# Kernel optimization log

Hardware: AMD Instinct MI355X
Metric: run time of the kernel (lower is better)

## Reference

```python
import jax, jax.numpy as jnp
import numpy as np

DIM = 768
HEADS = 12
HEAD_DIM = DIM // HEADS
SCALE = HEAD_DIM ** -0.5
LN_EPS = 1e-5


def setup_inputs() -> dict:
    key = jax.random.key(0)
    ks = jax.random.split(key, 12)
    B, N, C = 8, 1024, DIM
    g = (6.0 / (C + 3 * C)) ** 0.5  # xavier_uniform bound for qkv
    gp = (6.0 / (C + C)) ** 0.5     # xavier_uniform bound for proj
    return {
        "x": jax.random.normal(ks[0], (B, N, C), jnp.float32),
        "w_qkv_id": jax.random.uniform(ks[1], (3 * C, C), jnp.float32, -g, g),
        "w_qkv_cloth": jax.random.uniform(ks[2], (3 * C, C), jnp.float32, -g, g),
        "w_proj_id": jax.random.uniform(ks[3], (C, C), jnp.float32, -gp, gp),
        "b_proj_id": jnp.zeros((C,), jnp.float32),
        "w_proj_cloth": jax.random.uniform(ks[4], (C, C), jnp.float32, -gp, gp),
        "b_proj_cloth": jnp.zeros((C,), jnp.float32),
        "ln_id_w": jnp.ones((C,), jnp.float32),
        "ln_id_b": jnp.zeros((C,), jnp.float32),
        "ln_cloth_w": jnp.ones((C,), jnp.float32),
        "ln_cloth_b": jnp.zeros((C,), jnp.float32),
        "orth_scale": jnp.asarray(0.1, jnp.float32),
    }


def _layernorm(x, w, b):
    mu = jnp.mean(x, axis=-1, keepdims=True)
    var = jnp.var(x, axis=-1, keepdims=True)
    return (x - mu) * jax.lax.rsqrt(var + LN_EPS) * w + b


def _split_heads(qkv, B, N):
    qkv = qkv.reshape(B, N, 3, HEADS, HEAD_DIM).transpose(2, 0, 3, 1, 4)
    return qkv[0], qkv[1], qkv[2]


def _attn(q, k, v):
    s = jnp.einsum("bhnd,bhmd->bhnm", q, k) * SCALE
    s = jnp.clip(s, -20.0, 20.0)
    a = jax.nn.softmax(s, axis=-1)
    a = jnp.where(jnp.isnan(a), jnp.zeros_like(a), a)  # nan guard (dropout = eval/identity)
    return jnp.einsum("bhnm,bhmd->bhnd", a, v)


def reference(x, w_qkv_id, w_qkv_cloth, w_proj_id, b_proj_id, w_proj_cloth,
              b_proj_cloth, ln_id_w, ln_id_b, ln_cloth_w, ln_cloth_b, orth_scale):
    B, N, C = x.shape
    q_id, k_id, v_id = _split_heads(x @ w_qkv_id.T, B, N)
    q_cl, k_cl, v_cl = _split_heads(x @ w_qkv_cloth.T, B, N)

    # Gram-Schmidt orthogonal projection of q_id against q_cloth
    dot = jnp.sum(q_id * q_cl, axis=-1, keepdims=True)          # [B,H,N,1]
    norm_sq = jnp.sum(q_cl * q_cl, axis=-1, keepdims=True) + 1e-5
    coeff = jnp.clip(dot / norm_sq, -1.0, 1.0)
    scale = jnp.clip(orth_scale, 0.0, 1.0)
    q_id_ortho = q_id - scale * (coeff * q_cl)
    saliency = jnp.clip(jnp.mean(jnp.abs(dot) / jnp.sqrt(norm_sq), axis=1), 0.0, 1.0)  # [B,N,1]

    out_id = _attn(q_id_ortho, k_id, v_id).transpose(0, 2, 1, 3).reshape(B, N, C)
    out_cl = _attn(q_cl, k_cl, v_cl).transpose(0, 2, 1, 3).reshape(B, N, C)

    id_feat = _layernorm(out_id @ w_proj_id.T + b_proj_id, ln_id_w, ln_id_b)
    cl_feat = _layernorm(out_cl @ w_proj_cloth.T + b_proj_cloth, ln_cloth_w, ln_cloth_b)
    return id_feat, cl_feat, saliency
```

## Files before the change

kernel.cpp:

```cpp
#include <hip/hip_runtime.h>

typedef unsigned short u16;
typedef short s16x8 __attribute__((ext_vector_type(8)));
typedef float f32x4 __attribute__((ext_vector_type(4)));

#define DEV __device__ __forceinline__

#if __has_builtin(__builtin_amdgcn_exp2f)
#define EXP2F(x) __builtin_amdgcn_exp2f(x)
#else
#define EXP2F(x) exp2f(x)
#endif

DEV u16 f2bf(float f) {
  unsigned int u = __float_as_uint(f);
  u = (u + 0x7fffu + ((u >> 16) & 1u)) >> 16;
  return (u16)u;
}
DEV float bf2f(u16 h) { return __uint_as_float(((unsigned int)h) << 16); }
DEV unsigned int pk_trunc(float lo, float hi) {
  return __builtin_amdgcn_perm(__float_as_uint(hi), __float_as_uint(lo), 0x07060302u);
}

DEV void g2l16(const void* g, void* l) {
  __builtin_amdgcn_global_load_lds(
      (const __attribute__((address_space(1))) unsigned int*)g,
      (__attribute__((address_space(3))) unsigned int*)l, 16, 0, 0);
}

#define SPLANE 6291456

#define BAR __builtin_amdgcn_s_barrier()
#define WAIT_VM(n) asm volatile("s_waitcnt vmcnt(" #n ")" ::: "memory")
#define WAIT_LGKM0 asm volatile("s_waitcnt lgkmcnt(0)" ::: "memory")
#define PRIO1 __builtin_amdgcn_s_setprio(1)
#define PRIO0 __builtin_amdgcn_s_setprio(0)

__global__ __launch_bounds__(256) void k_cvt(const float* __restrict__ x,
                                             const float* __restrict__ wqi,
                                             const float* __restrict__ wqc,
                                             const float* __restrict__ wpi,
                                             const float* __restrict__ wpc,
                                             u16* __restrict__ xb,
                                             u16* __restrict__ wqkv,
                                             u16* __restrict__ wproj) {
  int i = blockIdx.x * 256 + threadIdx.x;
  const float* src; u16* dst; int off;
  if (i < 1572864)      { src = x;   dst = xb;             off = 0; }
  else if (i < 2015232) { src = wqi; dst = wqkv;           off = 1572864; }
  else if (i < 2457600) { src = wqc; dst = wqkv + 1769472; off = 2015232; }
  else if (i < 2605056) { src = wpi; dst = wproj;          off = 2457600; }
  else                  { src = wpc; dst = wproj + 589824; off = 2605056; }
  int j = i - off;
  float4 v = ((const float4*)src)[j];
  ushort4 o;
  o.x = f2bf(v.x); o.y = f2bf(v.y); o.z = f2bf(v.z); o.w = f2bf(v.w);
  ((ushort4*)dst)[j] = o;
}


DEV void qstg(const u16* pX, const u16* pW, int koff, u16* lA, u16* lB, int wave) {
#pragma unroll
  for (int it = 0; it < 4; ++it) {
    int rb = wave * 32 + it * 8;
    g2l16(pX + koff + it * (8 * 768), &lA[rb * 64]);
    g2l16(pW + koff + it * (8 * 768), &lB[rb * 64]);
  }
}

DEV void qcomp(const u16* lA, const u16* lB, int wr, int wc, int fr, int fq,
               f32x4 (&acc)[4][4]) {
#pragma unroll
  for (int ks = 0; ks < 2; ++ks) {
    s16x8 af[4], bfr[4];
#pragma unroll
    for (int i = 0; i < 4; i++) {
      int row = wc + i * 16 + fr;
      af[i] = *(const s16x8*)&lB[row * 64 + (((ks * 4 + fq) ^ (row & 7)) * 8)];
    }
#pragma unroll
    for (int j = 0; j < 4; j++) {
      int row = wr + j * 16 + fr;
      bfr[j] = *(const s16x8*)&lA[row * 64 + (((ks * 4 + fq) ^ (row & 7)) * 8)];
    }
    PRIO1;
#pragma unroll
    for (int i = 0; i < 4; i++)
#pragma unroll
      for (int j = 0; j < 4; j++)
        acc[i][j] = __builtin_amdgcn_mfma_f32_16x16x32_bf16(af[i], bfr[j], acc[i][j], 0, 0, 0);
    PRIO0;
  }
}

__global__ __launch_bounds__(256, 2) void k_qkv_gemm(const u16* __restrict__ X,
                                                     const u16* __restrict__ Wq,
                                                     u16* __restrict__ QK,
                                                     u16* __restrict__ VT) {
  __shared__ __align__(16) u16 sm[32768];

  const int idx = blockIdx.x;
  const int swz = (idx & 7) * 288 + (idx >> 3);
  const int bx = swz % 18;
  const int rem = swz / 18;
  const int by = rem & 63;
  const int z = rem >> 6;
  const int n0 = bx * 128, m0 = by * 128;

  const int tid = threadIdx.x;
  const int wave = tid >> 6, lane = tid & 63;
  const int wr = (wave >> 1) * 64, wc = (wave & 1) * 64;
  const int fr = lane & 15, fq = lane >> 4;

  const int srow = lane >> 3;
  const int scol = ((lane & 7) ^ srow) * 8;

  const u16* pX = X + (size_t)(m0 + wave * 32 + srow) * 768 + scol;
  const u16* pW = Wq + (size_t)z * (2304 * 768) + (size_t)(n0 + wave * 32 + srow) * 768 + scol;

  u16* const lA0 = sm;
  u16* const lB0 = sm + 8192;
  u16* const lA1 = sm + 16384;
  u16* const lB1 = sm + 24576;

  f32x4 acc[4][4];
#pragma unroll
  for (int i = 0; i < 4; i++)
#pragma unroll
    for (int j = 0; j < 4; j++) acc[i][j] = (f32x4){0.f, 0.f, 0.f, 0.f};

  qstg(pX, pW, 0, lA0, lB0, wave);
  qstg(pX, pW, 64, lA1, lB1, wave);
  WAIT_VM(8);
  BAR;

  const u16* pX2 = pX + 128;
  const u16* pW2 = pW + 128;

#pragma unroll
  for (int ii = 0; ii < 6; ++ii) {
    qcomp(lA0, lB0, wr, wc, fr, fq, acc);
    BAR;
    if (ii < 5) {
      qstg(pX2, pW2, 0, lA0, lB0, wave);
      WAIT_VM(8);
    } else {
      WAIT_VM(0);
    }
    BAR;
    qcomp(lA1, lB1, wr, wc, fr, fq, acc);
    BAR;
    if (ii < 5) {
      qstg(pX2, pW2, 64, lA1, lB1, wave);
      WAIT_VM(8);
      pX2 += 128; pW2 += 128;
    }
    BAR;
  }

  __syncthreads();
  u16* ep = sm + wave * 4608;
#pragma unroll
  for (int i = 0; i < 4; i++)
#pragma unroll
    for (int j = 0; j < 4; j++) {
      unsigned int lo = (unsigned int)f2bf(acc[i][j][0]) | ((unsigned int)f2bf(acc[i][j][1]) << 16);
      unsigned int hi = (unsigned int)f2bf(acc[i][j][2]) | ((unsigned int)f2bf(acc[i][j][3]) << 16);
      uint2 pk; pk.x = lo; pk.y = hi;
      *(uint2*)&ep[(j * 16 + fr) * 72 + i * 16 + fq * 4] = pk;
    }
  __builtin_amdgcn_s_waitcnt(0);

  const int c0 = n0 + wc;
  const int t0 = m0 + wr;
  const int b = t0 >> 10, tt0 = t0 & 1023;
  if (c0 < 1536) {
    const int three = (c0 >= 768) ? 1 : 0;
    const int h = (c0 - three * 768) >> 6;
    u16* dst = QK + ((size_t)z * 2 + three) * SPLANE +
               ((size_t)(b * 12 + h) * 1024 + tt0) * 64;
#pragma unroll
    for (int pass = 0; pass < 8; ++pass) {
      int row = pass * 8 + (lane >> 3);
      int dch = (lane & 7) * 8;
      *(uint4*)&dst[(size_t)row * 64 + dch] = *(const uint4*)&ep[row * 72 + dch];
    }
  } else {
    const int h = (c0 - 1536) >> 6;
    u16* dst = VT + (size_t)z * SPLANE + ((size_t)(b * 12 + h) * 64) * 1024 + tt0;
#pragma unroll
    for (int pass = 0; pass < 8; ++pass) {
      int d = pass * 8 + (lane >> 3);
      int tch = (lane & 7) * 8;
      unsigned int w0[4];
#pragma unroll
      for (int k2 = 0; k2 < 4; k2++) {
        unsigned int lo = ep[(tch + k2 * 2) * 72 + d];
        unsigned int hi = ep[(tch + k2 * 2 + 1) * 72 + d];
        w0[k2] = lo | (hi << 16);
      }
      uint4 val;
      val.x = w0[0]; val.y = w0[1]; val.z = w0[2]; val.w = w0[3];
      *(uint4*)&dst[(size_t)d * 1024 + tch] = val;
    }
  }
}

__global__ __launch_bounds__(256) void k_ortho(u16* __restrict__ QK,
                                               const float* __restrict__ orth_scale,
                                               float* __restrict__ sal) {
  const int wave = threadIdx.x >> 6, lane = threadIdx.x & 63;
  const int row = blockIdx.x * 4 + wave;
  const int b = row >> 10, n = row & 1023;
  const float scale = fminf(fmaxf(orth_scale[0], 0.f), 1.f);
  u16* qid = QK;
  u16* qcl = QK + (size_t)2 * SPLANE;
  float sacc = 0.f;
  for (int h = 0; h < 12; ++h) {
    size_t off = (((size_t)(b * 12 + h)) * 1024 + n) * 64 + lane;
    float qi = bf2f(qid[off]);
    float qc = bf2f(qcl[off]);
    float d = qi * qc, nq = qc * qc;
#pragma unroll
    for (int s = 1; s < 64; s <<= 1) { d += __shfl_xor(d, s); nq += __shfl_xor(nq, s); }
    nq += 1e-5f;
    float coeff = fminf(fmaxf(d / nq, -1.f), 1.f);
    qid[off] = f2bf(qi - scale * coeff * qc);
    sacc += fabsf(d) / sqrtf(nq);
  }
  if (lane == 0) sal[row] = fminf(fmaxf(sacc * (1.f / 12.f), 0.f), 1.f);
}

#define AST 72
#define PST 40
__global__ __launch_bounds__(256, 3) void k_attn(const u16* __restrict__ QK,
                                                 const u16* __restrict__ VT,
                                                 u16* __restrict__ aout) {
  __shared__ __align__(16) u16 sm[19456];
  u16* lK = sm;
  u16* lVT = sm + 4608;
  const int lid = blockIdx.x;
  const int swz = (lid & 7) * 96 + (lid >> 3);
  const int qb = swz & 3;
  const int pr = swz >> 2;
  const int z = pr / 96, bh = pr - (pr / 96) * 96;
  const int q0 = qb * 256;
  const int b = bh / 12, hd = bh - b * 12;
  const size_t plane = (size_t)bh * 65536;
  const u16* Q  = QK + (size_t)z * 2 * SPLANE + plane;
  const u16* K  = QK + ((size_t)z * 2 + 1) * SPLANE + plane;
  const u16* Vt = VT + (size_t)z * SPLANE + plane;

  const int tid = threadIdx.x, wave = tid >> 6, lane = tid & 63;
  const int fr = lane & 15, fq = lane >> 4;
  u16* lP = sm + 9216 + wave * 2560;

  s16x8 qf[4][2];
#pragma unroll
  for (int s = 0; s < 4; s++) {
    const u16* qrow = Q + (size_t)(q0 + wave * 64 + s * 16 + fr) * 64;
    qf[s][0] = *(const s16x8*)&qrow[fq * 8];
    qf[s][1] = *(const s16x8*)&qrow[32 + fq * 8];
  }

  f32x4 oacc[4][4];
  float lsum[4];
#pragma unroll
  for (int s = 0; s < 4; s++) {
    lsum[s] = 0.f;
#pragma unroll
    for (int j = 0; j < 4; j++) oacc[s][j] = (f32x4){0.f, 0.f, 0.f, 0.f};
  }

  const int srow = tid >> 3, sc8 = (tid & 7) * 8;

  uint4 rk0 = *(const uint4*)&K[(size_t)srow * 64 + sc8];
  uint4 rk1 = *(const uint4*)&K[(size_t)(srow + 32) * 64 + sc8];
  uint4 rv0 = *(const uint4*)&Vt[(size_t)srow * 1024 + sc8];
  uint4 rv1 = *(const uint4*)&Vt[(size_t)(srow + 32) * 1024 + sc8];

  for (int kv0 = 0; kv0 < 1024; kv0 += 64) {
    __syncthreads();
    *(uint4*)&lK[srow * AST + sc8]         = rk0;
    *(uint4*)&lK[(srow + 32) * AST + sc8]  = rk1;
    *(uint4*)&lVT[srow * AST + sc8]        = rv0;
    *(uint4*)&lVT[(srow + 32) * AST + sc8] = rv1;
    __syncthreads();

    {
      int nxt = (kv0 + 64) & 1023;
      const u16* kb = K + (size_t)nxt * 64;
      rk0 = *(const uint4*)&kb[(size_t)srow * 64 + sc8];
      rk1 = *(const uint4*)&kb[(size_t)(srow + 32) * 64 + sc8];
      const u16* vb = Vt + nxt;
      rv0 = *(const uint4*)&vb[(size_t)srow * 1024 + sc8];
      rv1 = *(const uint4*)&vb[(size_t)(srow + 32) * 1024 + sc8];
    }

#pragma unroll
    for (int ph = 0; ph < 2; ++ph) {
#pragma unroll
      for (int jh = 0; jh < 2; ++jh) {
        const int jt = ph * 2 + jh;
        s16x8 kf0 = *(const s16x8*)&lK[(jt * 16 + fr) * AST + fq * 8];
        s16x8 kf1 = *(const s16x8*)&lK[(jt * 16 + fr) * AST + 32 + fq * 8];
#pragma unroll
        for (int s = 0; s < 4; s++) {
          f32x4 t = (f32x4){0.f, 0.f, 0.f, 0.f};
          t = __builtin_amdgcn_mfma_f32_16x16x32_bf16(kf0, qf[s][0], t, 0, 0, 0);
          t = __builtin_amdgcn_mfma_f32_16x16x32_bf16(kf1, qf[s][1], t, 0, 0, 0);
          float p0 = EXP2F(fmaf(t[0], 0.18033688f, -28.8539008f));
          float p1 = EXP2F(fmaf(t[1], 0.18033688f, -28.8539008f));
          float p2 = EXP2F(fmaf(t[2], 0.18033688f, -28.8539008f));
          float p3 = EXP2F(fmaf(t[3], 0.18033688f, -28.8539008f));
          lsum[s] += (p0 + p1) + (p2 + p3);
          uint2 pk; pk.x = pk_trunc(p0, p1); pk.y = pk_trunc(p2, p3);
          *(uint2*)&lP[(s * 16 + fr) * PST + jh * 16 + fq * 4] = pk;
        }
      }
      WAIT_LGKM0;
      s16x8 pa[4];
#pragma unroll
      for (int s = 0; s < 4; s++) pa[s] = *(const s16x8*)&lP[(s * 16 + fr) * PST + fq * 8];
#pragma unroll
      for (int jt = 0; jt < 4; jt++) {
        s16x8 vb = *(const s16x8*)&lVT[(jt * 16 + fr) * AST + ph * 32 + fq * 8];
#pragma unroll
        for (int s = 0; s < 4; s++)
          oacc[s][jt] = __builtin_amdgcn_mfma_f32_16x16x32_bf16(pa[s], vb, oacc[s][jt], 0, 0, 0);
      }
    }
  }

#pragma unroll
  for (int s = 0; s < 4; s++) {
    float v = lsum[s];
    v += __shfl_xor(v, 16);
    v += __shfl_xor(v, 32);
    lsum[s] = v;
  }
#pragma unroll
  for (int s = 0; s < 4; s++) {
#pragma unroll
    for (int r = 0; r < 4; r++) {
      float inv = 1.f / __shfl(lsum[s], fq * 4 + r);
      int t = q0 + wave * 64 + s * 16 + fq * 4 + r;
      size_t base = ((size_t)z * 8192 + b * 1024 + t) * 768 + hd * 64 + fr;
#pragma unroll
      for (int jt = 0; jt < 4; jt++)
        aout[base + jt * 16] = f2bf(oacc[s][jt][r] * inv);
    }
  }
}

__global__ __launch_bounds__(256) void k_proj_gemm(const u16* __restrict__ A,
                                                   const u16* __restrict__ Wp,
                                                   const float* __restrict__ bias_id,
                                                   const float* __restrict__ bias_cl,
                                                   u16* __restrict__ out) {
  __shared__ __align__(16) u16 sm[18432];
  u16* lA = sm;
  u16* lB = sm + 8192;
  const int idx = blockIdx.x;
  const int swz = (idx & 7) * 96 + (idx >> 3);
  const int bx = swz % 6;
  const int rem = swz / 6;
  const int by = rem & 63;
  const int z = rem >> 6;
  const int n0 = bx * 128, m0 = by * 128;
  const u16* Az = A + (size_t)z * 8192 * 768;
  const u16* Wz = Wp + (size_t)z * 768 * 768;
  const float* bias = z ? bias_cl : bias_id;
  u16* oz = out + (size_t)z * 8192 * 768;
  const int tid = threadIdx.x;
  const int wave = tid >> 6, lane = tid & 63;
  const int wr = (wave >> 1) * 64, wc = (wave & 1) * 64;
  const int fr = lane & 15, fq = lane >> 4;

  float bv[4][4];
#pragma unroll
  for (int i = 0; i < 4; i++)
#pragma unroll
    for (int r = 0; r < 4; r++) bv[i][r] = bias[n0 + wc + i * 16 + fq * 4 + r];

  f32x4 acc[4][4];
#pragma unroll
  for (int i = 0; i < 4; i++)
#pragma unroll
    for (int j = 0; j < 4; j++) acc[i][j] = (f32x4){0.f, 0.f, 0.f, 0.f};

  const int srow = lane >> 3;
  const int scol = ((lane & 7) ^ srow) * 8;

  const u16* pAz = Az + (size_t)(m0 + wave * 32 + srow) * 768 + scol;
  const u16* pWz = Wz + (size_t)(n0 + wave * 32 + srow) * 768 + scol;

  for (int k0 = 0; k0 < 768; k0 += 64) {
    __syncthreads();
#pragma unroll
    for (int it = 0; it < 4; ++it) {
      int rb = wave * 32 + it * 8;
      g2l16(pAz + it * (8 * 768) + k0, &lA[rb * 64]);
      g2l16(pWz + it * (8 * 768) + k0, &lB[rb * 64]);
    }
    __syncthreads();
#pragma unroll
    for (int ks = 0; ks < 2; ++ks) {
      s16x8 af[4], bfr[4];
#pragma unroll
      for (int i = 0; i < 4; i++) {
        int row = wc + i * 16 + fr;
        af[i] = *(const s16x8*)&lB[row * 64 + (((ks * 4 + fq) ^ (row & 7)) * 8)];
      }
#pragma unroll
      for (int j = 0; j < 4; j++) {
        int row = wr + j * 16 + fr;
        bfr[j] = *(const s16x8*)&lA[row * 64 + (((ks * 4 + fq) ^ (row & 7)) * 8)];
      }
#pragma unroll
      for (int i = 0; i < 4; i++)
#pragma unroll
        for (int j = 0; j < 4; j++)
          acc[i][j] = __builtin_amdgcn_mfma_f32_16x16x32_bf16(af[i], bfr[j], acc[i][j], 0, 0, 0);
    }
  }

  __syncthreads();
  u16* ep = sm + wave * 4608;
#pragma unroll
  for (int i = 0; i < 4; i++)
#pragma unroll
    for (int j = 0; j < 4; j++) {
      unsigned int lo = (unsigned int)f2bf(acc[i][j][0] + bv[i][0]) |
                        ((unsigned int)f2bf(acc[i][j][1] + bv[i][1]) << 16);
      unsigned int hi = (unsigned int)f2bf(acc[i][j][2] + bv[i][2]) |
                        ((unsigned int)f2bf(acc[i][j][3] + bv[i][3]) << 16);
      uint2 pk; pk.x = lo; pk.y = hi;
      *(uint2*)&ep[(j * 16 + fr) * 72 + i * 16 + fq * 4] = pk;
    }
  __builtin_amdgcn_s_waitcnt(0);

  const int c0 = n0 + wc;
#pragma unroll
  for (int pass = 0; pass < 8; ++pass) {
    int row = pass * 8 + (lane >> 3);
    int dch = (lane & 7) * 8;
    u16* dst = oz + (size_t)(m0 + wr + row) * 768 + c0;
    *(uint4*)&dst[dch] = *(const uint4*)&ep[row * 72 + dch];
  }
}

__global__ __launch_bounds__(256) void k_ln(const u16* __restrict__ pin,
                                            const float* __restrict__ w_id,
                                            const float* __restrict__ b_id,
                                            const float* __restrict__ w_cl,
                                            const float* __restrict__ b_cl,
                                            float* __restrict__ out) {
  __shared__ float red[2][8];
  const int row = blockIdx.x;
  const int z = row >> 13;
  const float* w = z ? w_cl : w_id;
  const float* bb = z ? b_cl : b_id;
  const u16* x = pin + (size_t)row * 768;
  float v[3];
  float s = 0.f, s2 = 0.f;
#pragma unroll
  for (int i = 0; i < 3; i++) {
    v[i] = bf2f(x[threadIdx.x + i * 256]);
    s += v[i];
    s2 += v[i] * v[i];
  }
#pragma unroll
  for (int sh = 1; sh < 64; sh <<= 1) { s += __shfl_xor(s, sh); s2 += __shfl_xor(s2, sh); }
  const int wave = threadIdx.x >> 6, lane = threadIdx.x & 63;
  if (lane == 0) { red[0][wave] = s; red[1][wave] = s2; }
  __syncthreads();
  s = red[0][0] + red[0][1] + red[0][2] + red[0][3];
  s2 = red[1][0] + red[1][1] + red[1][2] + red[1][3];
  float mu = s * (1.f / 768.f);
  float var = s2 * (1.f / 768.f) - mu * mu;
  float rstd = rsqrtf(fmaxf(var, 0.f) + 1e-5f);
  float* o = out + (size_t)row * 768;
#pragma unroll
  for (int i = 0; i < 3; i++) {
    int c = threadIdx.x + i * 256;
    o[c] = (v[i] - mu) * rstd * w[c] + bb[c];
  }
}

extern "C" void kernel_launch(void* const* d_in, const int* in_sizes, int n_in,
                              void* d_out, int out_size, void* d_ws, size_t ws_size,
                              hipStream_t stream) {
  const float* x        = (const float*)d_in[0];
  const float* w_qkv_id = (const float*)d_in[1];
  const float* w_qkv_cl = (const float*)d_in[2];
  const float* w_proj_id= (const float*)d_in[3];
  const float* b_proj_id= (const float*)d_in[4];
  const float* w_proj_cl= (const float*)d_in[5];
  const float* b_proj_cl= (const float*)d_in[6];
  const float* ln_id_w  = (const float*)d_in[7];
  const float* ln_id_b  = (const float*)d_in[8];
  const float* ln_cl_w  = (const float*)d_in[9];
  const float* ln_cl_b  = (const float*)d_in[10];
  const float* orth     = (const float*)d_in[11];
  float* out = (float*)d_out;

  u16* xb    = (u16*)d_ws;
  u16* wqkv  = xb + 6291456;
  u16* wproj = wqkv + 3538944;
  u16* qk    = wproj + 1179648;
  u16* vt    = qk + 25165824;
  u16* aout  = vt + 12582912;
  u16* pout  = qk;

  k_cvt<<<10752, 256, 0, stream>>>(x, w_qkv_id, w_qkv_cl, w_proj_id, w_proj_cl,
                                   xb, wqkv, wproj);
  k_qkv_gemm<<<2304, 256, 0, stream>>>(xb, wqkv, qk, vt);
  k_ortho<<<2048, 256, 0, stream>>>(qk, orth, out + 12582912);
  k_attn<<<768, 256, 0, stream>>>(qk, vt, aout);
  k_proj_gemm<<<768, 256, 0, stream>>>(aout, wproj, b_proj_id, b_proj_cl, pout);
  k_ln<<<16384, 256, 0, stream>>>(pout, ln_id_w, ln_id_b, ln_cl_w, ln_cl_b, out);
}
```

Measured before the change: 311.9 us.

## Fuse Gram-Schmidt orthogonalization into attention kernel and drop ortho pass

Removes the standalone k_ortho kernel. The q_id projection against q_cloth is now computed in registers inside k_attn after Q is loaded, and saliency is accumulated per head through atomicAdd. Saliency is zeroed in the QKV GEMM and scaled and clamped in the projection GEMM. The V-transpose epilogue is also rewritten to store transposed into shared memory with a padded stride so the global writes become straight vector copies. The goal is to save a launch plus a full read/write pass over q_id and q_cloth, at the cost of atomics and extra Q_cloth loads in the z==0 attention blocks.

New measurement: 279.1 us, median of 2. -10.5%, faster.

```diff
diff --git a/kernel.cpp b/kernel.cpp
--- a/kernel.cpp
+++ b/kernel.cpp
@@ -96,10 +96,14 @@
 __global__ __launch_bounds__(256, 2) void k_qkv_gemm(const u16* __restrict__ X,
                                                      const u16* __restrict__ Wq,
                                                      u16* __restrict__ QK,
-                                                     u16* __restrict__ VT) {
+                                                     u16* __restrict__ VT,
+                                                     float* __restrict__ sal) {
   __shared__ __align__(16) u16 sm[32768];
 
   const int idx = blockIdx.x;
+  const int tid = threadIdx.x;
+  if (idx < 32) sal[idx * 256 + tid] = 0.f;
+
   const int swz = (idx & 7) * 288 + (idx >> 3);
   const int bx = swz % 18;
   const int rem = swz / 18;
@@ -107,7 +111,6 @@
   const int z = rem >> 6;
   const int n0 = bx * 128, m0 = by * 128;
 
-  const int tid = threadIdx.x;
   const int wave = tid >> 6, lane = tid & 63;
   const int wr = (wave >> 1) * 64, wc = (wave & 1) * 64;
   const int fr = lane & 15, fq = lane >> 4;
@@ -159,22 +162,21 @@
   }
 
   __syncthreads();
-  u16* ep = sm + wave * 4608;
-#pragma unroll
-  for (int i = 0; i < 4; i++)
-#pragma unroll
-    for (int j = 0; j < 4; j++) {
-      unsigned int lo = (unsigned int)f2bf(acc[i][j][0]) | ((unsigned int)f2bf(acc[i][j][1]) << 16);
-      unsigned int hi = (unsigned int)f2bf(acc[i][j][2]) | ((unsigned int)f2bf(acc[i][j][3]) << 16);
-      uint2 pk; pk.x = lo; pk.y = hi;
-      *(uint2*)&ep[(j * 16 + fr) * 72 + i * 16 + fq * 4] = pk;
-    }
-  __builtin_amdgcn_s_waitcnt(0);
-
   const int c0 = n0 + wc;
   const int t0 = m0 + wr;
   const int b = t0 >> 10, tt0 = t0 & 1023;
   if (c0 < 1536) {
+    u16* ep = sm + wave * 4608;
+#pragma unroll
+    for (int i = 0; i < 4; i++)
+#pragma unroll
+      for (int j = 0; j < 4; j++) {
+        unsigned int lo = (unsigned int)f2bf(acc[i][j][0]) | ((unsigned int)f2bf(acc[i][j][1]) << 16);
+        unsigned int hi = (unsigned int)f2bf(acc[i][j][2]) | ((unsigned int)f2bf(acc[i][j][3]) << 16);
+        uint2 pk; pk.x = lo; pk.y = hi;
+        *(uint2*)&ep[(j * 16 + fr) * 72 + i * 16 + fq * 4] = pk;
+      }
+    __builtin_amdgcn_s_waitcnt(0);
     const int three = (c0 >= 768) ? 1 : 0;
     const int h = (c0 - three * 768) >> 6;
     u16* dst = QK + ((size_t)z * 2 + three) * SPLANE +
@@ -188,53 +190,30 @@
   } else {
     const int h = (c0 - 1536) >> 6;
     u16* dst = VT + (size_t)z * SPLANE + ((size_t)(b * 12 + h) * 64) * 1024 + tt0;
+    u16* ep2 = sm + wave * 5632;
+#pragma unroll
+    for (int i = 0; i < 4; i++)
+#pragma unroll
+      for (int j = 0; j < 4; j++)
+#pragma unroll
+        for (int r = 0; r < 4; r++)
+          ep2[(i * 16 + fq * 4 + r) * 88 + j * 16 + fr] = f2bf(acc[i][j][r]);
+    __builtin_amdgcn_s_waitcnt(0);
 #pragma unroll
     for (int pass = 0; pass < 8; ++pass) {
       int d = pass * 8 + (lane >> 3);
       int tch = (lane & 7) * 8;
-      unsigned int w0[4];
-#pragma unroll
-      for (int k2 = 0; k2 < 4; k2++) {
-        unsigned int lo = ep[(tch + k2 * 2) * 72 + d];
-        unsigned int hi = ep[(tch + k2 * 2 + 1) * 72 + d];
-        w0[k2] = lo | (hi << 16);
-      }
-      uint4 val;
-      val.x = w0[0]; val.y = w0[1]; val.z = w0[2]; val.w = w0[3];
-      *(uint4*)&dst[(size_t)d * 1024 + tch] = val;
-    }
-  }
-}
-
-__global__ __launch_bounds__(256) void k_ortho(u16* __restrict__ QK,
-                                               const float* __restrict__ orth_scale,
-                                               float* __restrict__ sal) {
-  const int wave = threadIdx.x >> 6, lane = threadIdx.x & 63;
-  const int row = blockIdx.x * 4 + wave;
-  const int b = row >> 10, n = row & 1023;
-  const float scale = fminf(fmaxf(orth_scale[0], 0.f), 1.f);
-  u16* qid = QK;
-  u16* qcl = QK + (size_t)2 * SPLANE;
-  float sacc = 0.f;
-  for (int h = 0; h < 12; ++h) {
-    size_t off = (((size_t)(b * 12 + h)) * 1024 + n) * 64 + lane;
-    float qi = bf2f(qid[off]);
-    float qc = bf2f(qcl[off]);
-    float d = qi * qc, nq = qc * qc;
-#pragma unroll
-    for (int s = 1; s < 64; s <<= 1) { d += __shfl_xor(d, s); nq += __shfl_xor(nq, s); }
-    nq += 1e-5f;
-    float coeff = fminf(fmaxf(d / nq, -1.f), 1.f);
-    qid[off] = f2bf(qi - scale * coeff * qc);
-    sacc += fabsf(d) / sqrtf(nq);
-  }
-  if (lane == 0) sal[row] = fminf(fmaxf(sacc * (1.f / 12.f), 0.f), 1.f);
+      *(uint4*)&dst[(size_t)d * 1024 + tch] = *(const uint4*)&ep2[d * 88 + tch];
+    }
+  }
 }
 
 #define AST 72
 #define PST 40
 __global__ __launch_bounds__(256, 3) void k_attn(const u16* __restrict__ QK,
                                                  const u16* __restrict__ VT,
+                                                 const float* __restrict__ orth_scale,
+                                                 float* __restrict__ sal,
                                                  u16* __restrict__ aout) {
   __shared__ __align__(16) u16 sm[19456];
   u16* lK = sm;
@@ -263,6 +242,37 @@
     qf[s][1] = *(const s16x8*)&qrow[32 + fq * 8];
   }
 
+  if (z == 0) {
+    const float scale = fminf(fmaxf(orth_scale[0], 0.f), 1.f);
+    const u16* Qc = QK + (size_t)2 * SPLANE + plane;
+#pragma unroll
+    for (int s = 0; s < 4; s++) {
+      const u16* qcrow = Qc + (size_t)(q0 + wave * 64 + s * 16 + fr) * 64;
+      s16x8 qc0 = *(const s16x8*)&qcrow[fq * 8];
+      s16x8 qc1 = *(const s16x8*)&qcrow[32 + fq * 8];
+      float d = 0.f, nq = 0.f;
+#pragma unroll
+      for (int e = 0; e < 8; e++) {
+        float a0 = bf2f((u16)qf[s][0][e]), a1 = bf2f((u16)qf[s][1][e]);
+        float c0 = bf2f((u16)qc0[e]),      c1 = bf2f((u16)qc1[e]);
+        d  = fmaf(a0, c0, fmaf(a1, c1, d));
+        nq = fmaf(c0, c0, fmaf(c1, c1, nq));
+      }
+      d += __shfl_xor(d, 16);  d += __shfl_xor(d, 32);
+      nq += __shfl_xor(nq, 16); nq += __shfl_xor(nq, 32);
+      nq += 1e-5f;
+      float coeff = fminf(fmaxf(d / nq, -1.f), 1.f);
+      float sc = scale * coeff;
+#pragma unroll
+      for (int e = 0; e < 8; e++) {
+        qf[s][0][e] = (short)f2bf(bf2f((u16)qf[s][0][e]) - sc * bf2f((u16)qc0[e]));
+        qf[s][1][e] = (short)f2bf(bf2f((u16)qf[s][1][e]) - sc * bf2f((u16)qc1[e]));
+      }
+      if (lane < 16)
+        atomicAdd(&sal[b * 1024 + q0 + wave * 64 + s * 16 + fr], fabsf(d) / sqrtf(nq));
+    }
+  }
+
   f32x4 oacc[4][4];
   float lsum[4];
 #pragma unroll
@@ -357,11 +367,18 @@
                                                    const u16* __restrict__ Wp,
                                                    const float* __restrict__ bias_id,
                                                    const float* __restrict__ bias_cl,
+                                                   float* __restrict__ sal,
                                                    u16* __restrict__ out) {
   __shared__ __align__(16) u16 sm[18432];
   u16* lA = sm;
   u16* lB = sm + 8192;
   const int idx = blockIdx.x;
+  const int tid = threadIdx.x;
+  if (idx < 32) {
+    int i2 = idx * 256 + tid;
+    float v = sal[i2] * (1.f / 12.f);
+    sal[i2] = fminf(fmaxf(v, 0.f), 1.f);
+  }
   const int swz = (idx & 7) * 96 + (idx >> 3);
   const int bx = swz % 6;
   const int rem = swz / 6;
@@ -372,7 +389,6 @@
   const u16* Wz = Wp + (size_t)z * 768 * 768;
   const float* bias = z ? bias_cl : bias_id;
   u16* oz = out + (size_t)z * 8192 * 768;
-  const int tid = threadIdx.x;
   const int wave = tid >> 6, lane = tid & 63;
   const int wr = (wave >> 1) * 64, wc = (wave & 1) * 64;
   const int fr = lane & 15, fq = lane >> 4;
@@ -504,6 +520,7 @@
   const float* ln_cl_b  = (const float*)d_in[10];
   const float* orth     = (const float*)d_in[11];
   float* out = (float*)d_out;
+  float* sal = out + 12582912;
 
   u16* xb    = (u16*)d_ws;
   u16* wqkv  = xb + 6291456;
@@ -515,9 +532,8 @@
 
   k_cvt<<<10752, 256, 0, stream>>>(x, w_qkv_id, w_qkv_cl, w_proj_id, w_proj_cl,
                                    xb, wqkv, wproj);
-  k_qkv_gemm<<<2304, 256, 0, stream>>>(xb, wqkv, qk, vt);
-  k_ortho<<<2048, 256, 0, stream>>>(qk, orth, out + 12582912);
-  k_attn<<<768, 256, 0, stream>>>(qk, vt, aout);
-  k_proj_gemm<<<768, 256, 0, stream>>>(aout, wproj, b_proj_id, b_proj_cl, pout);
+  k_qkv_gemm<<<2304, 256, 0, stream>>>(xb, wqkv, qk, vt, sal);
+  k_attn<<<768, 256, 0, stream>>>(qk, vt, orth, sal, aout);
+  k_proj_gemm<<<768, 256, 0, stream>>>(aout, wproj, b_proj_id, b_proj_cl, sal, pout);
   k_ln<<<16384, 256, 0, stream>>>(pout, ln_id_w, ln_id_b, ln_cl_w, ln_cl_b, out);
 }
```
